# Kernel tuning notes

Measured on AMD Instinct MI355X. Metric: run time of the kernel, lower is better.

## Reference

```python
import jax, jax.numpy as jnp
import numpy as np

TEMPERATURE = 0.5
BATCH_SIZE = 4096
EPS = 1e-8  # torch.nn.CosineSimilarity default eps


def setup_inputs() -> dict:
    key = jax.random.key(0)
    k1, k2 = jax.random.split(key)
    z1 = jax.random.normal(k1, (BATCH_SIZE, 256), dtype=jnp.float32)
    z2 = jax.random.normal(k2, (BATCH_SIZE, 256), dtype=jnp.float32)
    return {"z1": z1, "z2": z2}


def reference(z1, z2):
    B = z1.shape[0]
    N = 2 * B
    reps = jnp.concatenate([z1, z2], axis=0)  # [N, D]
    # Cosine similarity (torch clamps each norm to eps before dividing)
    norms = jnp.maximum(jnp.linalg.norm(reps, axis=1, keepdims=True), EPS)
    z = reps / norms
    sim = z @ z.T  # [N, N] cosine similarity matrix

    # positives: diagonals at offsets +B and -B (they are identical by symmetry,
    # but keep the original concat order: [diag(+B), diag(-B)])
    l_pos = jnp.diagonal(sim, offset=B)
    r_pos = jnp.diagonal(sim, offset=-B)
    positives = jnp.concatenate([l_pos, r_pos])  # [N]

    inv_t = 1.0 / TEMPERATURE
    pos_logit = positives * inv_t  # logits[:, 0]

    # negatives are all off-diagonal entries of each row (the positive pair is
    # thus present twice in the logits, faithful to the original). CE with
    # label 0 => loss_i = logsumexp(logits_i) - logits_i[0].
    neg_logits = jnp.where(jnp.eye(N, dtype=bool), -jnp.inf, sim * inv_t)
    lse = jnp.logaddexp(pos_logit, jax.scipy.special.logsumexp(neg_logits, axis=1))
    loss = jnp.sum(lse - pos_logit) / N
    return loss
```

## Files before the change

### kernel.cpp

```cpp
#include <hip/hip_runtime.h>
#include <hip/hip_bf16.h>
#include <cstdint>
#include <cstddef>
#include <math.h>

#define BSZ   4096
#define NROW  8192
#define DIM   256
#define INV_T 2.0f
#define EPS_N 1e-8f

typedef __attribute__((ext_vector_type(8))) short bf16x8;
typedef __attribute__((ext_vector_type(4))) float f32x4;

__device__ __forceinline__ unsigned short f2bf(float x) {
    __hip_bfloat16 h = __float2bfloat16(x);
    return __builtin_bit_cast(unsigned short, h);
}

__device__ __forceinline__ void load_lds16(const void* g, void* l) {
    __builtin_amdgcn_global_load_lds(
        (const __attribute__((address_space(1))) void*)g,
        (__attribute__((address_space(3))) void*)l,
        16, 0, 0);
}

__global__ __launch_bounds__(256)
void nt_normalize(const float* __restrict__ z1,
                  const float* __restrict__ z2,
                  __hip_bfloat16* __restrict__ zn,
                  float* __restrict__ rowsum) {
    const int wave = threadIdx.x >> 6;
    const int lane = threadIdx.x & 63;
    const int row  = blockIdx.x * 4 + wave;
    const float* src = (row < BSZ) ? (z1 + (size_t)row * DIM)
                                   : (z2 + (size_t)(row - BSZ) * DIM);
    const float4 v = ((const float4*)src)[lane];
    float ss = v.x * v.x + v.y * v.y + v.z * v.z + v.w * v.w;
    #pragma unroll
    for (int off = 32; off; off >>= 1) ss += __shfl_xor(ss, off);
    const float rinv = 1.0f / fmaxf(sqrtf(ss), EPS_N);
    ushort4 o;
    o.x = f2bf(v.x * rinv);
    o.y = f2bf(v.y * rinv);
    o.z = f2bf(v.z * rinv);
    o.w = f2bf(v.w * rinv);
    ((ushort4*)(zn + (size_t)row * DIM))[lane] = o;
    if (lane == 0) rowsum[row] = 0.0f;
}

__global__ __launch_bounds__(256)
void nt_gram(const __hip_bfloat16* __restrict__ zn,
             float* __restrict__ rowsum,
             float* __restrict__ pos) {
    const int l = blockIdx.x;
    int bi = (int)((129.0 - sqrt(16641.0 - 8.0 * (double)l)) * 0.5);
    while (64 * (bi + 1) - (bi + 1) * bi / 2 <= l) ++bi;
    while (64 * bi - bi * (bi - 1) / 2 > l) --bi;
    const int bj = bi + (l - (64 * bi - bi * (bi - 1) / 2));

    __shared__ __hip_bfloat16 As[128 * 64];
    __shared__ __hip_bfloat16 Bs[128 * 64];

    const int t    = threadIdx.x;
    const int lane = t & 63;
    const int wave = t >> 6;
    const int wrow = (wave >> 1) * 64;
    const int wcol = (wave & 1) * 64;

    f32x4 acc[4][4] = {};

    const __hip_bfloat16* Ag = zn + (size_t)bi * 128 * DIM;
    const __hip_bfloat16* Bg = zn + (size_t)bj * 128 * DIM;

    const int srow = t >> 3;
    const int sc   = (t & 7) ^ (srow & 7);

    const int q   = lane >> 4;
    const int r16 = lane & 15;
    const int sw  = r16 & 7;

    for (int k0 = 0; k0 < DIM; k0 += 64) {
        #pragma unroll
        for (int p = 0; p < 4; ++p) {
            const int row = p * 32 + srow;
            load_lds16(Ag + (size_t)row * DIM + k0 + sc * 8,
                       (char*)As + p * 4096 + t * 16);
            load_lds16(Bg + (size_t)row * DIM + k0 + sc * 8,
                       (char*)Bs + p * 4096 + t * 16);
        }
        __syncthreads();

        #pragma unroll
        for (int kk = 0; kk < 64; kk += 32) {
            const int cc = (kk >> 3) + q;
            const int cpos = (cc ^ sw) << 4;
            bf16x8 af[4], bfr[4];
            #pragma unroll
            for (int mi = 0; mi < 4; ++mi) {
                const int m = wrow + mi * 16 + r16;
                af[mi] = *(const bf16x8*)((const char*)As + m * 128 + cpos);
            }
            #pragma unroll
            for (int ni = 0; ni < 4; ++ni) {
                const int n = wcol + ni * 16 + r16;
                bfr[ni] = *(const bf16x8*)((const char*)Bs + n * 128 + cpos);
            }
            #pragma unroll
            for (int mi = 0; mi < 4; ++mi)
                #pragma unroll
                for (int ni = 0; ni < 4; ++ni)
                    acc[mi][ni] = __builtin_amdgcn_mfma_f32_16x16x32_bf16(
                        af[mi], bfr[ni], acc[mi][ni], 0, 0, 0);
        }
        __syncthreads();
    }

    const int c = lane & 15;
    const bool diag_block = (bi == bj);
    float colp[4] = {0.f, 0.f, 0.f, 0.f};

    #pragma unroll
    for (int mi = 0; mi < 4; ++mi) {
        #pragma unroll
        for (int r = 0; r < 4; ++r) {
            const int grow = bi * 128 + wrow + mi * 16 + q * 4 + r;
            float s = 0.f;
            #pragma unroll
            for (int ni = 0; ni < 4; ++ni) {
                const int gcol = bj * 128 + wcol + ni * 16 + c;
                const float val = acc[mi][ni][r];
                float e = __expf(val * INV_T);
                e = (grow == gcol) ? 0.f : e;
                s += e;
                colp[ni] += e;
                if (gcol == grow + BSZ) {
                    pos[grow] = val;
                    pos[gcol] = val;
                }
            }
            s += __shfl_xor(s, 1);
            s += __shfl_xor(s, 2);
            s += __shfl_xor(s, 4);
            s += __shfl_xor(s, 8);
            if (c == 0) atomicAdd(&rowsum[grow], s);
        }
    }
    if (!diag_block) {
        #pragma unroll
        for (int ni = 0; ni < 4; ++ni) {
            float cs = colp[ni];
            cs += __shfl_xor(cs, 16);
            cs += __shfl_xor(cs, 32);
            if (q == 0) atomicAdd(&rowsum[bj * 128 + wcol + ni * 16 + c], cs);
        }
    }
}

__global__ __launch_bounds__(1024)
void nt_finalize(const float* __restrict__ rowsum,
                 const float* __restrict__ pos,
                 float* __restrict__ out) {
    float v = 0.f;
    for (int i = threadIdx.x; i < NROW; i += 1024) {
        const float pl = pos[i] * INV_T;
        v += logf(__expf(pl) + rowsum[i]) - pl;
    }
    #pragma unroll
    for (int off = 32; off; off >>= 1) v += __shfl_xor(v, off);
    __shared__ float red[16];
    if ((threadIdx.x & 63) == 0) red[threadIdx.x >> 6] = v;
    __syncthreads();
    if (threadIdx.x == 0) {
        float s = 0.f;
        #pragma unroll
        for (int w = 0; w < 16; ++w) s += red[w];
        out[0] = s * (1.0f / NROW);
    }
}

extern "C" void kernel_launch(void* const* d_in, const int* in_sizes, int n_in,
                              void* d_out, int out_size, void* d_ws, size_t ws_size,
                              hipStream_t stream) {
    const float* z1 = (const float*)d_in[0];
    const float* z2 = (const float*)d_in[1];
    float* out = (float*)d_out;

    __hip_bfloat16* zn = (__hip_bfloat16*)d_ws;
    float* rowsum = (float*)((char*)d_ws + (size_t)NROW * DIM * 2);
    float* pos    = rowsum + NROW;

    nt_normalize<<<NROW / 4, 256, 0, stream>>>(z1, z2, zn, rowsum);
    nt_gram<<<2080, 256, 0, stream>>>(zn, rowsum, pos);
    nt_finalize<<<1, 1024, 0, stream>>>(rowsum, pos, out);
}
```

Before: 107.2 us.

## Use 256x256 triangular tiles with double-buffered LDS and block-local row sums

Grows the Gram tile from 128x128 to 256x256, using 512 threads and 8x4 MFMA fragments per wave. Double-buffers the LDS stages so loads for the next K slice overlap compute on the current one. Reorders the triangular block index so consecutive blocks share row bands. Row and column exp-sums are first reduced in LDS and then written with one global atomic per row. The aim is fewer global loads and atomics and better L2 locality, at the cost of 128KB of LDS per block and higher register pressure, which limits occupancy.

```diff
diff --git a/kernel.cpp b/kernel.cpp
--- a/kernel.cpp
+++ b/kernel.cpp
@@ -49,86 +49,113 @@
     if (lane == 0) rowsum[row] = 0.0f;
 }
 
-__global__ __launch_bounds__(256)
+__global__ __launch_bounds__(512, 2)
 void nt_gram(const __hip_bfloat16* __restrict__ zn,
              float* __restrict__ rowsum,
              float* __restrict__ pos) {
-    const int l = blockIdx.x;
-    int bi = (int)((129.0 - sqrt(16641.0 - 8.0 * (double)l)) * 0.5);
-    while (64 * (bi + 1) - (bi + 1) * bi / 2 <= l) ++bi;
-    while (64 * bi - bi * (bi - 1) / 2 > l) --bi;
-    const int bj = bi + (l - (64 * bi - bi * (bi - 1) / 2));
-
-    __shared__ __hip_bfloat16 As[128 * 64];
-    __shared__ __hip_bfloat16 Bs[128 * 64];
+    __shared__ char lds[131072];
+
+    const int bidx = blockIdx.x;
+    const int l = (bidx & 7) * 66 + (bidx >> 3);
+    int b = 0;
+    #pragma unroll
+    for (int bb = 1; bb < 8; ++bb)
+        if (l >= 130 * bb - 8 * bb * bb) b = bb;
+    const int idx = l - (130 * b - 8 * b * b);
+    int bi, bj;
+    if (idx < 10) {
+        const int j0   = (idx >= 6) ? 3 : (idx >= 3) ? 2 : (idx >= 1) ? 1 : 0;
+        const int toff = (j0 == 3) ? 6 : (j0 == 2) ? 3 : (j0 == 1) ? 1 : 0;
+        bi = 4 * b + idx - toff;
+        bj = 4 * b + j0;
+    } else {
+        bi = 4 * b + ((idx - 10) & 3);
+        bj = 4 * b + 4 + ((idx - 10) >> 2);
+    }
 
     const int t    = threadIdx.x;
     const int lane = t & 63;
     const int wave = t >> 6;
-    const int wrow = (wave >> 1) * 64;
-    const int wcol = (wave & 1) * 64;
-
-    f32x4 acc[4][4] = {};
-
-    const __hip_bfloat16* Ag = zn + (size_t)bi * 128 * DIM;
-    const __hip_bfloat16* Bg = zn + (size_t)bj * 128 * DIM;
+    const int wrow = (wave >> 2) * 128;
+    const int wcol = (wave & 3) * 64;
+
+    const __hip_bfloat16* Ag = zn + (size_t)bi * 256 * DIM;
+    const __hip_bfloat16* Bg = zn + (size_t)bj * 256 * DIM;
+
+    char* A0 = lds;
+    char* B0 = lds + 32768;
+    char* A1 = lds + 65536;
+    char* B1 = lds + 98304;
 
     const int srow = t >> 3;
     const int sc   = (t & 7) ^ (srow & 7);
-
-    const int q   = lane >> 4;
-    const int r16 = lane & 15;
-    const int sw  = r16 & 7;
-
-    for (int k0 = 0; k0 < DIM; k0 += 64) {
+    const int q    = lane >> 4;
+    const int r16  = lane & 15;
+    const int sw   = r16 & 7;
+
+    f32x4 acc[8][4] = {};
+
+    auto STAGE = [&](int k0, char* As, char* Bs) {
         #pragma unroll
         for (int p = 0; p < 4; ++p) {
-            const int row = p * 32 + srow;
-            load_lds16(Ag + (size_t)row * DIM + k0 + sc * 8,
-                       (char*)As + p * 4096 + t * 16);
-            load_lds16(Bg + (size_t)row * DIM + k0 + sc * 8,
-                       (char*)Bs + p * 4096 + t * 16);
-        }
-        __syncthreads();
-
+            const int row = p * 64 + srow;
+            load_lds16(Ag + (size_t)row * DIM + k0 + sc * 8, As + p * 8192 + t * 16);
+            load_lds16(Bg + (size_t)row * DIM + k0 + sc * 8, Bs + p * 8192 + t * 16);
+        }
+    };
+
+    auto COMPUTE = [&](const char* As, const char* Bs) {
         #pragma unroll
         for (int kk = 0; kk < 64; kk += 32) {
-            const int cc = (kk >> 3) + q;
+            const int cc   = (kk >> 3) + q;
             const int cpos = (cc ^ sw) << 4;
-            bf16x8 af[4], bfr[4];
-            #pragma unroll
-            for (int mi = 0; mi < 4; ++mi) {
-                const int m = wrow + mi * 16 + r16;
-                af[mi] = *(const bf16x8*)((const char*)As + m * 128 + cpos);
-            }
-            #pragma unroll
-            for (int ni = 0; ni < 4; ++ni) {
-                const int n = wcol + ni * 16 + r16;
-                bfr[ni] = *(const bf16x8*)((const char*)Bs + n * 128 + cpos);
-            }
-            #pragma unroll
-            for (int mi = 0; mi < 4; ++mi)
+            bf16x8 af[8], bfr[4];
+            #pragma unroll
+            for (int mi = 0; mi < 8; ++mi)
+                af[mi] = *(const bf16x8*)(As + (wrow + mi * 16 + r16) * 128 + cpos);
+            #pragma unroll
+            for (int ni = 0; ni < 4; ++ni)
+                bfr[ni] = *(const bf16x8*)(Bs + (wcol + ni * 16 + r16) * 128 + cpos);
+            #pragma unroll
+            for (int mi = 0; mi < 8; ++mi)
                 #pragma unroll
                 for (int ni = 0; ni < 4; ++ni)
                     acc[mi][ni] = __builtin_amdgcn_mfma_f32_16x16x32_bf16(
                         af[mi], bfr[ni], acc[mi][ni], 0, 0, 0);
         }
-        __syncthreads();
-    }
-
-    const int c = lane & 15;
+    };
+
+    STAGE(0, A0, B0);
+    __syncthreads();
+    STAGE(64, A1, B1);
+    COMPUTE(A0, B0);
+    __syncthreads();
+    STAGE(128, A0, B0);
+    COMPUTE(A1, B1);
+    __syncthreads();
+    STAGE(192, A1, B1);
+    COMPUTE(A0, B0);
+    __syncthreads();
+    float* rowacc = (float*)A0;
+    float* colacc = (float*)(A0 + 1024);
+    ((float*)A0)[t] = 0.0f;
+    COMPUTE(A1, B1);
+    __syncthreads();
+
+    const int  c          = r16;
     const bool diag_block = (bi == bj);
     float colp[4] = {0.f, 0.f, 0.f, 0.f};
 
     #pragma unroll
-    for (int mi = 0; mi < 4; ++mi) {
+    for (int mi = 0; mi < 8; ++mi) {
         #pragma unroll
         for (int r = 0; r < 4; ++r) {
-            const int grow = bi * 128 + wrow + mi * 16 + q * 4 + r;
+            const int trow = wrow + mi * 16 + q * 4 + r;
+            const int grow = bi * 256 + trow;
             float s = 0.f;
             #pragma unroll
             for (int ni = 0; ni < 4; ++ni) {
-                const int gcol = bj * 128 + wcol + ni * 16 + c;
+                const int gcol = bj * 256 + wcol + ni * 16 + c;
                 const float val = acc[mi][ni][r];
                 float e = __expf(val * INV_T);
                 e = (grow == gcol) ? 0.f : e;
@@ -143,7 +170,7 @@
             s += __shfl_xor(s, 2);
             s += __shfl_xor(s, 4);
             s += __shfl_xor(s, 8);
-            if (c == 0) atomicAdd(&rowsum[grow], s);
+            if (c == 0) atomicAdd(&rowacc[trow], s);
         }
     }
     if (!diag_block) {
@@ -152,8 +179,14 @@
             float cs = colp[ni];
             cs += __shfl_xor(cs, 16);
             cs += __shfl_xor(cs, 32);
-            if (q == 0) atomicAdd(&rowsum[bj * 128 + wcol + ni * 16 + c], cs);
-        }
+            if (q == 0) atomicAdd(&colacc[wcol + ni * 16 + c], cs);
+        }
+    }
+    __syncthreads();
+    if (t < 256) {
+        atomicAdd(&rowsum[bi * 256 + t], rowacc[t]);
+    } else if (!diag_block) {
+        atomicAdd(&rowsum[bj * 256 + (t - 256)], colacc[t - 256]);
     }
 }
 
@@ -191,6 +224,6 @@
     float* pos    = rowsum + NROW;
 
     nt_normalize<<<NROW / 4, 256, 0, stream>>>(z1, z2, zn, rowsum);
-    nt_gram<<<2080, 256, 0, stream>>>(zn, rowsum, pos);
+    nt_gram<<<528, 512, 0, stream>>>(zn, rowsum, pos);
     nt_finalize<<<1, 1024, 0, stream>>>(rowsum, pos, out);
 }
```

Measured after the change: 111.5 us. 4.0% more time.

## Load Gram tile fragments directly from global into registers, reduce row sums in LDS

Applied to the files above, without the earlier changes.

The Gram kernel no longer stages A/B tiles in shared memory. Each lane now loads its MFMA fragments straight from global memory into registers, double-buffered across the K dimension, so the staging copies and barriers go away. Block indices are remapped so that consecutive blocks spread across the triangular tile space, which changes cache and XCD locality. Row and column partial sums are first combined in shared memory, then written with one global atomic per row, cutting global atomic traffic. The cost is that each fragment is read from global/L2 by several waves with no LDS reuse, and the per-lane 16-byte loads are strided by row, which may lower load efficiency.

```diff
diff --git a/kernel.cpp b/kernel.cpp
--- a/kernel.cpp
+++ b/kernel.cpp
@@ -16,13 +16,6 @@
 __device__ __forceinline__ unsigned short f2bf(float x) {
     __hip_bfloat16 h = __float2bfloat16(x);
     return __builtin_bit_cast(unsigned short, h);
-}
-
-__device__ __forceinline__ void load_lds16(const void* g, void* l) {
-    __builtin_amdgcn_global_load_lds(
-        (const __attribute__((address_space(1))) void*)g,
-        (__attribute__((address_space(3))) void*)l,
-        16, 0, 0);
 }
 
 __global__ __launch_bounds__(256)
@@ -53,70 +46,65 @@
 void nt_gram(const __hip_bfloat16* __restrict__ zn,
              float* __restrict__ rowsum,
              float* __restrict__ pos) {
-    const int l = blockIdx.x;
+    const int bid = blockIdx.x;
+    const int l = (bid & 7) * 260 + (bid >> 3);
     int bi = (int)((129.0 - sqrt(16641.0 - 8.0 * (double)l)) * 0.5);
     while (64 * (bi + 1) - (bi + 1) * bi / 2 <= l) ++bi;
     while (64 * bi - bi * (bi - 1) / 2 > l) --bi;
     const int bj = bi + (l - (64 * bi - bi * (bi - 1) / 2));
-
-    __shared__ __hip_bfloat16 As[128 * 64];
-    __shared__ __hip_bfloat16 Bs[128 * 64];
 
     const int t    = threadIdx.x;
     const int lane = t & 63;
     const int wave = t >> 6;
     const int wrow = (wave >> 1) * 64;
     const int wcol = (wave & 1) * 64;
+    const int q    = lane >> 4;
+    const int r16  = lane & 15;
+
+    const char* pa = (const char*)zn + ((size_t)bi * 128 + wrow + r16) * 512 + q * 16;
+    const char* pb = (const char*)zn + ((size_t)bj * 128 + wcol + r16) * 512 + q * 16;
 
     f32x4 acc[4][4] = {};
+    bf16x8 a0[4], b0[4], a1[4], b1[4];
 
-    const __hip_bfloat16* Ag = zn + (size_t)bi * 128 * DIM;
-    const __hip_bfloat16* Bg = zn + (size_t)bj * 128 * DIM;
+    auto LOADF = [&](bf16x8* A, bf16x8* B, int kb) {
+        #pragma unroll
+        for (int mi = 0; mi < 4; ++mi)
+            A[mi] = *(const bf16x8*)(pa + mi * 8192 + kb);
+        #pragma unroll
+        for (int ni = 0; ni < 4; ++ni)
+            B[ni] = *(const bf16x8*)(pb + ni * 8192 + kb);
+    };
+    auto MF = [&](bf16x8* A, bf16x8* B) {
+        #pragma unroll
+        for (int mi = 0; mi < 4; ++mi)
+            #pragma unroll
+            for (int ni = 0; ni < 4; ++ni)
+                acc[mi][ni] = __builtin_amdgcn_mfma_f32_16x16x32_bf16(
+                    A[mi], B[ni], acc[mi][ni], 0, 0, 0);
+    };
 
-    const int srow = t >> 3;
-    const int sc   = (t & 7) ^ (srow & 7);
+    LOADF(a0, b0, 0);
+    int kb = 64;
+    #pragma unroll 1
+    for (int it = 0; it < 3; ++it) {
+        LOADF(a1, b1, kb);
+        MF(a0, b0);
+        LOADF(a0, b0, kb + 64);
+        MF(a1, b1);
+        kb += 128;
+    }
+    LOADF(a1, b1, 448);
+    MF(a0, b0);
+    MF(a1, b1);
 
-    const int q   = lane >> 4;
-    const int r16 = lane & 15;
-    const int sw  = r16 & 7;
+    __shared__ float red[256];
+    red[t] = 0.0f;
+    __syncthreads();
+    float* rowacc = red;
+    float* colacc = red + 128;
 
-    for (int k0 = 0; k0 < DIM; k0 += 64) {
-        #pragma unroll
-        for (int p = 0; p < 4; ++p) {
-            const int row = p * 32 + srow;
-            load_lds16(Ag + (size_t)row * DIM + k0 + sc * 8,
-                       (char*)As + p * 4096 + t * 16);
-            load_lds16(Bg + (size_t)row * DIM + k0 + sc * 8,
-                       (char*)Bs + p * 4096 + t * 16);
-        }
-        __syncthreads();
-
-        #pragma unroll
-        for (int kk = 0; kk < 64; kk += 32) {
-            const int cc = (kk >> 3) + q;
-            const int cpos = (cc ^ sw) << 4;
-            bf16x8 af[4], bfr[4];
-            #pragma unroll
-            for (int mi = 0; mi < 4; ++mi) {
-                const int m = wrow + mi * 16 + r16;
-                af[mi] = *(const bf16x8*)((const char*)As + m * 128 + cpos);
-            }
-            #pragma unroll
-            for (int ni = 0; ni < 4; ++ni) {
-                const int n = wcol + ni * 16 + r16;
-                bfr[ni] = *(const bf16x8*)((const char*)Bs + n * 128 + cpos);
-            }
-            #pragma unroll
-            for (int mi = 0; mi < 4; ++mi)
-                #pragma unroll
-                for (int ni = 0; ni < 4; ++ni)
-                    acc[mi][ni] = __builtin_amdgcn_mfma_f32_16x16x32_bf16(
-                        af[mi], bfr[ni], acc[mi][ni], 0, 0, 0);
-        }
-        __syncthreads();
-    }
-
-    const int c = lane & 15;
+    const int  c          = r16;
     const bool diag_block = (bi == bj);
     float colp[4] = {0.f, 0.f, 0.f, 0.f};
 
@@ -124,7 +112,8 @@
     for (int mi = 0; mi < 4; ++mi) {
         #pragma unroll
         for (int r = 0; r < 4; ++r) {
-            const int grow = bi * 128 + wrow + mi * 16 + q * 4 + r;
+            const int trow = wrow + mi * 16 + q * 4 + r;
+            const int grow = bi * 128 + trow;
             float s = 0.f;
             #pragma unroll
             for (int ni = 0; ni < 4; ++ni) {
@@ -143,7 +132,7 @@
             s += __shfl_xor(s, 2);
             s += __shfl_xor(s, 4);
             s += __shfl_xor(s, 8);
-            if (c == 0) atomicAdd(&rowsum[grow], s);
+            if (c == 0) atomicAdd(&rowacc[trow], s);
         }
     }
     if (!diag_block) {
@@ -152,8 +141,14 @@
             float cs = colp[ni];
             cs += __shfl_xor(cs, 16);
             cs += __shfl_xor(cs, 32);
-            if (q == 0) atomicAdd(&rowsum[bj * 128 + wcol + ni * 16 + c], cs);
+            if (q == 0) atomicAdd(&colacc[wcol + ni * 16 + c], cs);
         }
+    }
+    __syncthreads();
+    if (t < 128) {
+        atomicAdd(&rowsum[bi * 128 + t], rowacc[t]);
+    } else if (!diag_block) {
+        atomicAdd(&rowsum[bj * 128 + (t - 128)], colacc[t - 128]);
     }
 }
 
```

Result: slower. 146.5 us (+36.6%).

## Pre-tile normalized embeddings into swizzled LDS-ready layout for contiguous gram loads

Applied to the files above, without the earlier changes.

The normalize kernel now writes bf16 rows into a blocked layout (128-row tiles, split into 64-wide k-chunks, with the XOR swizzle already applied), so each gram tile's k-chunk is one contiguous 16 KB region. The gram kernel then loads it with fully linear 16-byte global-to-LDS copies instead of strided per-row gathers. This aims to improve global memory coalescing and simplify address computation in the loads. In exchange, the normalize stores become scattered 8-byte writes.

```diff
diff --git a/kernel.cpp b/kernel.cpp
--- a/kernel.cpp
+++ b/kernel.cpp
@@ -28,7 +28,7 @@
 __global__ __launch_bounds__(256)
 void nt_normalize(const float* __restrict__ z1,
                   const float* __restrict__ z2,
-                  __hip_bfloat16* __restrict__ zn,
+                  char* __restrict__ zn2,
                   float* __restrict__ rowsum) {
     const int wave = threadIdx.x >> 6;
     const int lane = threadIdx.x & 63;
@@ -45,12 +45,18 @@
     o.y = f2bf(v.y * rinv);
     o.z = f2bf(v.z * rinv);
     o.w = f2bf(v.w * rinv);
-    ((ushort4*)(zn + (size_t)row * DIM))[lane] = o;
+    const int s    = row >> 7;
+    const int lrow = row & 127;
+    const int kc   = lane >> 4;
+    const int unit = (lane >> 1) & 7;
+    const int half = lane & 1;
+    const int u    = unit ^ (lrow & 7);
+    *(ushort4*)(zn2 + (size_t)s * 65536 + kc * 16384 + lrow * 128 + u * 16 + half * 8) = o;
     if (lane == 0) rowsum[row] = 0.0f;
 }
 
 __global__ __launch_bounds__(256)
-void nt_gram(const __hip_bfloat16* __restrict__ zn,
+void nt_gram(const char* __restrict__ zn2,
              float* __restrict__ rowsum,
              float* __restrict__ pos) {
     const int l = blockIdx.x;
@@ -59,53 +65,43 @@
     while (64 * bi - bi * (bi - 1) / 2 > l) --bi;
     const int bj = bi + (l - (64 * bi - bi * (bi - 1) / 2));
 
-    __shared__ __hip_bfloat16 As[128 * 64];
-    __shared__ __hip_bfloat16 Bs[128 * 64];
+    __shared__ char As[16384];
+    __shared__ char Bs[16384];
 
     const int t    = threadIdx.x;
     const int lane = t & 63;
     const int wave = t >> 6;
     const int wrow = (wave >> 1) * 64;
     const int wcol = (wave & 1) * 64;
+    const int q    = lane >> 4;
+    const int r16  = lane & 15;
+    const int sw   = r16 & 7;
+
+    const char* A2 = zn2 + (size_t)bi * 65536;
+    const char* B2 = zn2 + (size_t)bj * 65536;
 
     f32x4 acc[4][4] = {};
 
-    const __hip_bfloat16* Ag = zn + (size_t)bi * 128 * DIM;
-    const __hip_bfloat16* Bg = zn + (size_t)bj * 128 * DIM;
-
-    const int srow = t >> 3;
-    const int sc   = (t & 7) ^ (srow & 7);
-
-    const int q   = lane >> 4;
-    const int r16 = lane & 15;
-    const int sw  = r16 & 7;
-
-    for (int k0 = 0; k0 < DIM; k0 += 64) {
+    for (int kc = 0; kc < 4; ++kc) {
         #pragma unroll
-        for (int p = 0; p < 4; ++p) {
-            const int row = p * 32 + srow;
-            load_lds16(Ag + (size_t)row * DIM + k0 + sc * 8,
-                       (char*)As + p * 4096 + t * 16);
-            load_lds16(Bg + (size_t)row * DIM + k0 + sc * 8,
-                       (char*)Bs + p * 4096 + t * 16);
-        }
+        for (int p = 0; p < 4; ++p)
+            load_lds16(A2 + kc * 16384 + p * 4096 + t * 16, As + p * 4096 + t * 16);
+        #pragma unroll
+        for (int p = 0; p < 4; ++p)
+            load_lds16(B2 + kc * 16384 + p * 4096 + t * 16, Bs + p * 4096 + t * 16);
         __syncthreads();
 
         #pragma unroll
         for (int kk = 0; kk < 64; kk += 32) {
-            const int cc = (kk >> 3) + q;
+            const int cc   = (kk >> 3) + q;
             const int cpos = (cc ^ sw) << 4;
             bf16x8 af[4], bfr[4];
             #pragma unroll
-            for (int mi = 0; mi < 4; ++mi) {
-                const int m = wrow + mi * 16 + r16;
-                af[mi] = *(const bf16x8*)((const char*)As + m * 128 + cpos);
-            }
+            for (int mi = 0; mi < 4; ++mi)
+                af[mi] = *(const bf16x8*)(As + (wrow + mi * 16 + r16) * 128 + cpos);
             #pragma unroll
-            for (int ni = 0; ni < 4; ++ni) {
-                const int n = wcol + ni * 16 + r16;
-                bfr[ni] = *(const bf16x8*)((const char*)Bs + n * 128 + cpos);
-            }
+            for (int ni = 0; ni < 4; ++ni)
+                bfr[ni] = *(const bf16x8*)(Bs + (wcol + ni * 16 + r16) * 128 + cpos);
             #pragma unroll
             for (int mi = 0; mi < 4; ++mi)
                 #pragma unroll
@@ -116,7 +112,7 @@
         __syncthreads();
     }
 
-    const int c = lane & 15;
+    const int c = r16;
     const bool diag_block = (bi == bj);
     float colp[4] = {0.f, 0.f, 0.f, 0.f};
 
@@ -186,11 +182,11 @@
     const float* z2 = (const float*)d_in[1];
     float* out = (float*)d_out;
 
-    __hip_bfloat16* zn = (__hip_bfloat16*)d_ws;
+    char*  zn2    = (char*)d_ws;
     float* rowsum = (float*)((char*)d_ws + (size_t)NROW * DIM * 2);
     float* pos    = rowsum + NROW;
 
-    nt_normalize<<<NROW / 4, 256, 0, stream>>>(z1, z2, zn, rowsum);
-    nt_gram<<<2080, 256, 0, stream>>>(zn, rowsum, pos);
+    nt_normalize<<<NROW / 4, 256, 0, stream>>>(z1, z2, zn2, rowsum);
+    nt_gram<<<2080, 256, 0, stream>>>(zn2, rowsum, pos);
     nt_finalize<<<1, 1024, 0, stream>>>(rowsum, pos, out);
 }
```

After: 107.2 us. About the same (+0.0%).
